# Kernel tuning notes

Measured on AMD Instinct MI355X. Metric: run time of the kernel, lower is better.

## Reference

```python
import jax, jax.numpy as jnp
import numpy as np

N_NODES = 50000
N_EDGES = 800000
IN_DIM = 128
HIDDEN = 256
N_CLASSES = 16
N_GRAPHS = 128


def setup_inputs() -> dict:
    key = jax.random.key(0)
    ks = jax.random.split(key, 10)
    x = jax.random.normal(ks[0], (N_NODES, IN_DIM), dtype=jnp.float32)
    edge_index = jax.random.randint(ks[1], (2, N_EDGES), 0, N_NODES, dtype=jnp.int64)
    batch = jnp.sort(jax.random.randint(ks[2], (N_NODES,), 0, N_GRAPHS, dtype=jnp.int64))
    s = 1.0 / np.sqrt(HIDDEN)
    return {
        "x": x,
        "edge_index": edge_index,
        "batch": batch,
        "W_in": jax.random.normal(ks[3], (IN_DIM, HIDDEN), dtype=jnp.float32) / np.sqrt(IN_DIM),
        "b_in": jnp.zeros((HIDDEN,), dtype=jnp.float32),
        "W1": jax.random.normal(ks[4], (HIDDEN, HIDDEN), dtype=jnp.float32) * s,
        "b1": jnp.zeros((HIDDEN,), dtype=jnp.float32),
        "W2": jax.random.normal(ks[5], (HIDDEN, HIDDEN), dtype=jnp.float32) * s,
        "b2": jnp.zeros((HIDDEN,), dtype=jnp.float32),
        "W_out": jax.random.normal(ks[6], (HIDDEN, N_CLASSES), dtype=jnp.float32) * s,
        "b_out": jnp.zeros((N_CLASSES,), dtype=jnp.float32),
    }


def gcn_conv(x, W, b, src, dst):
    # PyG GCNConv: add self-loops, symmetric norm D^-1/2 A D^-1/2, scatter-add at target.
    h = x @ W  # [N, H]
    n = x.shape[0]
    # degree of target nodes, including one self-loop per node
    deg = jax.ops.segment_sum(jnp.ones_like(dst, dtype=h.dtype), dst, num_segments=n) + 1.0
    dinv = deg ** -0.5  # [N]
    norm = dinv[src] * dinv[dst]  # [E]
    msg = h[src] * norm[:, None]  # [E, H]  gather + scale
    agg = jax.ops.segment_sum(msg, dst, num_segments=n)  # scatter-add
    agg = agg + h * (dinv * dinv)[:, None]  # self-loop contribution
    return agg + b


def reference(x, edge_index, batch, W_in, b_in, W1, b1, W2, b2, W_out, b_out):
    src, dst = edge_index[0], edge_index[1]
    h = x @ W_in + b_in
    # layer 1 (dropout is identity in eval mode)
    h = jax.nn.relu(gcn_conv(h, W1, b1, src, dst))
    # layer 2
    h = jax.nn.relu(gcn_conv(h, W2, b2, src, dst))
    # global mean pool over graphs
    sums = jax.ops.segment_sum(h, batch, num_segments=N_GRAPHS)  # [G, H]
    counts = jax.ops.segment_sum(jnp.ones((h.shape[0],), h.dtype), batch, num_segments=N_GRAPHS)
    pooled = sums / jnp.maximum(counts, 1.0)[:, None]
    return pooled @ W_out + b_out  # [G, n_classes]
```

## Files before the change

kernel.cpp:

```cpp
#include <hip/hip_runtime.h>
#include <hip/hip_bf16.h>

typedef __attribute__((ext_vector_type(8))) short bf16x8;
typedef __attribute__((ext_vector_type(4))) float f32x4;
typedef __attribute__((ext_vector_type(8))) unsigned short u16x8;

__device__ __forceinline__ unsigned short f2bf(float f) {
    unsigned u = __float_as_uint(f);
    u += 0x7fff + ((u >> 16) & 1);
    return (unsigned short)(u >> 16);
}
__device__ __forceinline__ float bf2f(unsigned short s) {
    return __uint_as_float(((unsigned)s) << 16);
}

#define GL2LDS16(g, l) __builtin_amdgcn_global_load_lds(                      \
        (const __attribute__((address_space(1))) void*)(g),                   \
        (__attribute__((address_space(3))) void*)(l), 16, 0, 0)


__global__ __launch_bounds__(256) void fused_misc_kernel(
        const int* __restrict__ dst, int* __restrict__ cnt, int e,
        const float* __restrict__ W2, unsigned short* __restrict__ Wt2,
        const float* __restrict__ x, unsigned short* __restrict__ xb, int n4,
        int CB, int TB) {
    int b = blockIdx.x;
    if (b < CB) {
        int i = b * 256 + threadIdx.x;
        if (i < e) atomicAdd(&cnt[dst[i]], 1);
    } else if (b < CB + TB) {
        int i = (b - CB) * 256 + threadIdx.x;
        int k = i >> 8, n = i & 255;
        Wt2[(size_t)n * 256 + k] = f2bf(W2[i]);
    } else {
        int i = (b - CB - TB) * 256 + threadIdx.x;
        if (i < n4) {
            float4 v = ((const float4*)x)[i];
            ushort4 o;
            o.x = f2bf(v.x); o.y = f2bf(v.y); o.z = f2bf(v.z); o.w = f2bf(v.w);
            ((ushort4*)xb)[i] = o;
        }
    }
}


__global__ __launch_bounds__(256) void wfuse_kernel(const float* __restrict__ W_in,
                                                    const float* __restrict__ b_in,
                                                    const float* __restrict__ W1,
                                                    unsigned short* __restrict__ WfT,
                                                    float* __restrict__ bv) {
    __shared__ float row[256];
    int k = blockIdx.x;
    int n = threadIdx.x;
    row[n] = (k < 128) ? W_in[k * 256 + n] : b_in[n];
    __syncthreads();
    float acc = 0.f;
    #pragma unroll 4
    for (int j = 0; j < 256; ++j) acc = fmaf(row[j], W1[j * 256 + n], acc);
    if (k < 128) WfT[(size_t)n * 128 + k] = f2bf(acc);
    else bv[n] = acc;
}


__global__ __launch_bounds__(256) void block_sum_kernel(const int* __restrict__ cnt,
                                                        int* __restrict__ bsums, int n) {
    int tid = threadIdx.x;
    int i = blockIdx.x * 256 + tid;
    int v = (i < n) ? cnt[i] : 0;
    #pragma unroll
    for (int off = 32; off > 0; off >>= 1) v += __shfl_down(v, off);
    __shared__ int ws[4];
    if ((tid & 63) == 0) ws[tid >> 6] = v;
    __syncthreads();
    if (tid == 0) bsums[blockIdx.x] = ws[0] + ws[1] + ws[2] + ws[3];
}

__global__ __launch_bounds__(256) void scatter_scan_kernel(const int* __restrict__ cnt,
                                                           const int* __restrict__ bsums,
                                                           int* __restrict__ offsets,
                                                           int* __restrict__ cursor,
                                                           float* __restrict__ dinv,
                                                           int n, int nb) {
    int tid = threadIdx.x;
    int lane = tid & 63, wid = tid >> 6;
    __shared__ int ws[4], wp[4];

    int bv = (tid < nb && tid < (int)blockIdx.x) ? bsums[tid] : 0;
    int br = bv;
    #pragma unroll
    for (int off = 32; off > 0; off >>= 1) br += __shfl_down(br, off);
    if (lane == 0) wp[wid] = br;

    int i = blockIdx.x * 256 + tid;
    int v = (i < n) ? cnt[i] : 0;
    int s = v;
    #pragma unroll
    for (int off = 1; off < 64; off <<= 1) {
        int t = __shfl_up(s, off);
        if (lane >= off) s += t;
    }
    if (lane == 63) ws[wid] = s;
    __syncthreads();
    int wo = 0;
    #pragma unroll
    for (int k = 0; k < 4; ++k) wo += (k < wid) ? ws[k] : 0;
    int bpref = wp[0] + wp[1] + wp[2] + wp[3];
    int excl = bpref + wo + s - v;
    if (i <= n) { offsets[i] = excl; }
    if (i < n) {
        cursor[i] = excl;
        dinv[i] = rsqrtf((float)v + 1.0f);
    }
}

__global__ void fill_kernel(const int* __restrict__ src, const int* __restrict__ dst,
                            int* __restrict__ cursor, int* __restrict__ csr, int e) {
    int i = blockIdx.x * blockDim.x + threadIdx.x;
    if (i < e) {
        int p = atomicAdd(&cursor[dst[i]], 1);
        csr[p] = src[i];
    }
}


template <int MODE>
__global__ __launch_bounds__(256) void gemm_bf16(const unsigned short* __restrict__ A,
                                                 const unsigned short* __restrict__ Wt,
                                                 const float* __restrict__ aux,
                                                 const float* __restrict__ aux2,
                                                 const float* __restrict__ aux3,
                                                 unsigned short* __restrict__ C,
                                                 int M, int K) {
    __shared__ unsigned short As[128 * 64];
    __shared__ unsigned short Bs[128 * 64];
    const int tid  = threadIdx.x;
    const int lane = tid & 63;
    const int w    = tid >> 6;
    const int wr   = w >> 1, wc = w & 1;
    const int row0 = blockIdx.x * 128;
    const int col0 = blockIdx.y * 128;
    const int mlane = lane & 15, quad = lane >> 4;

    f32x4 acc[4][4];
    #pragma unroll
    for (int i = 0; i < 4; ++i)
        #pragma unroll
        for (int j = 0; j < 4; ++j) acc[i][j] = f32x4{0.f, 0.f, 0.f, 0.f};

    const unsigned short* gA[4]; const unsigned short* gB[4];
    unsigned short* lA[4]; unsigned short* lB[4];
    #pragma unroll
    for (int p = 0; p < 4; ++p) {
        int cid = (p * 4 + w) * 64 + lane;
        int row = cid >> 3, slot = cid & 7;
        int rowA = row0 + row; if (rowA >= M) rowA = M - 1;
        gA[p] = A + (size_t)rowA * K + slot * 8;
        gB[p] = Wt + (size_t)(col0 + row) * K + slot * 8;
        lA[p] = &As[((p * 4 + w) * 64) * 8];
        lB[p] = &Bs[((p * 4 + w) * 64) * 8];
    }

    for (int k0 = 0; k0 < K; k0 += 64) {
        #pragma unroll
        for (int p = 0; p < 4; ++p) GL2LDS16(gA[p] + k0, lA[p]);
        #pragma unroll
        for (int p = 0; p < 4; ++p) GL2LDS16(gB[p] + k0, lB[p]);
        __syncthreads();
        #pragma unroll
        for (int ks = 0; ks < 2; ++ks) {
            bf16x8 af[4], bfv[4];
            #pragma unroll
            for (int i = 0; i < 4; ++i)
                af[i] = *(const bf16x8*)&As[(wr * 64 + i * 16 + mlane) * 64 + ks * 32 + quad * 8];
            #pragma unroll
            for (int j = 0; j < 4; ++j)
                bfv[j] = *(const bf16x8*)&Bs[(wc * 64 + j * 16 + mlane) * 64 + ks * 32 + quad * 8];
            #pragma unroll
            for (int i = 0; i < 4; ++i)
                #pragma unroll
                for (int j = 0; j < 4; ++j)
                    acc[i][j] = __builtin_amdgcn_mfma_f32_16x16x32_bf16(af[i], bfv[j], acc[i][j], 0, 0, 0);
        }
        __syncthreads();
    }

    float bj[4], cj[4];
    if (MODE == 0) {
        #pragma unroll
        for (int j = 0; j < 4; ++j) bj[j] = aux[col0 + wc * 64 + j * 16 + mlane];
    } else if (MODE == 2) {
        #pragma unroll
        for (int j = 0; j < 4; ++j) {
            int gcol = col0 + wc * 64 + j * 16 + mlane;
            bj[j] = aux2[gcol];
            cj[j] = aux3[gcol];
        }
    }
    #pragma unroll
    for (int i = 0; i < 4; ++i) {
        #pragma unroll
        for (int r = 0; r < 4; ++r) {
            int grow = row0 + wr * 64 + i * 16 + quad * 4 + r;
            if (grow < M) {
                float d = (MODE != 0) ? aux[grow] : 0.f;
                #pragma unroll
                for (int j = 0; j < 4; ++j) {
                    int gcol = col0 + wc * 64 + j * 16 + mlane;
                    float v = acc[i][j][r];
                    if (MODE == 0)      v = v + bj[j];
                    else if (MODE == 1) v = v * d;
                    else {              v = fmaf(d, bj[j], v) + cj[j]; v = fmaxf(v, 0.f); }
                    C[(size_t)grow * 256 + gcol] = f2bf(v);
                }
            }
        }
    }
}


__global__ __launch_bounds__(256) void agg_x_kernel(const unsigned short* __restrict__ xb,
                                                    const int* __restrict__ offsets,
                                                    const int* __restrict__ csr,
                                                    const float* __restrict__ dinv,
                                                    unsigned short* __restrict__ ax,
                                                    float* __restrict__ s_out, int n) {
    int node = blockIdx.x * 4 + (threadIdx.x >> 6);
    if (node >= n) return;
    int lane = threadIdx.x & 63;
    int q = lane >> 4, hl = lane & 15;
    const u16x8* x8 = (const u16x8*)xb;
    int beg = offsets[node], end = offsets[node + 1];
    float dn = dinv[node];
    float acc[8] = {0.f,0.f,0.f,0.f,0.f,0.f,0.f,0.f};
    float acc2[8] = {0.f,0.f,0.f,0.f,0.f,0.f,0.f,0.f};
    float sdl = 0.f;

    int e = beg;
    while (e < end) {
        int cnt = end - e; if (cnt > 64) cnt = 64;
        int myi = 0; float mydv = 0.f;
        if (lane < cnt) { myi = csr[e + lane]; mydv = dinv[myi]; sdl += mydv; }
        for (int j = 0; j < cnt; j += 32) {
            int s[8]; float w[8]; u16x8 v[8];
            #pragma unroll
            for (int k = 0; k < 8; ++k) {
                int slot = j + 4 * k + q;
                s[k] = __shfl(myi, slot);
                w[k] = __shfl(mydv, slot);
            }
            #pragma unroll
            for (int k = 0; k < 8; ++k) v[k] = x8[(size_t)s[k] * 16 + hl];
            #pragma unroll
            for (int k = 0; k < 8; k += 2) {
                #pragma unroll
                for (int c = 0; c < 8; ++c) acc[c]  = fmaf(bf2f(v[k][c]),   w[k],   acc[c]);
                #pragma unroll
                for (int c = 0; c < 8; ++c) acc2[c] = fmaf(bf2f(v[k+1][c]), w[k+1], acc2[c]);
            }
        }
        e += cnt;
    }
    #pragma unroll
    for (int c = 0; c < 8; ++c) {
        acc[c] += acc2[c];
        acc[c] += __shfl_xor(acc[c], 16);
        acc[c] += __shfl_xor(acc[c], 32);
    }
    float sd = sdl;
    #pragma unroll
    for (int off = 32; off > 0; off >>= 1) sd += __shfl_down(sd, off);
    if (lane < 16) {
        u16x8 sv = x8[(size_t)node * 16 + hl];
        u16x8 r;
        #pragma unroll
        for (int c = 0; c < 8; ++c) {
            float v = fmaf(dn, bf2f(sv[c]), acc[c]) * dn;
            r[c] = f2bf(v);
        }
        ((u16x8*)ax)[(size_t)node * 16 + hl] = r;
        if (lane == 0) s_out[node] = dn * (sd + dn);
    }
}


__global__ __launch_bounds__(256) void agg_kernel(const unsigned short* __restrict__ hs,
                                                  const int* __restrict__ offsets,
                                                  const int* __restrict__ csr,
                                                  const float* __restrict__ dinv,
                                                  const float* __restrict__ bias,
                                                  unsigned short* __restrict__ out, int n) {
    int node = blockIdx.x * 4 + (threadIdx.x >> 6);
    if (node >= n) return;
    int lane = threadIdx.x & 63;
    int half = lane >> 5, hl = lane & 31;
    const u16x8* hs8 = (const u16x8*)hs;
    int beg = offsets[node], end = offsets[node + 1];
    float acc[8] = {0.f,0.f,0.f,0.f,0.f,0.f,0.f,0.f};
    float acc2[8] = {0.f,0.f,0.f,0.f,0.f,0.f,0.f,0.f};

    int e = beg;
    while (e < end) {
        int cnt = end - e; if (cnt > 64) cnt = 64;
        int myi = (lane < cnt) ? csr[e + lane] : 0;
        for (int j = 0; j < cnt; j += 16) {
            int s[8]; float w[8]; u16x8 v[8];
            #pragma unroll
            for (int k = 0; k < 8; ++k) {
                int slot = j + 2 * k + half;
                s[k] = __shfl(myi, slot);
                w[k] = (slot < cnt) ? 1.0f : 0.0f;
            }
            #pragma unroll
            for (int k = 0; k < 8; ++k) v[k] = hs8[(size_t)s[k] * 32 + hl];
            #pragma unroll
            for (int k = 0; k < 8; k += 2) {
                #pragma unroll
                for (int c = 0; c < 8; ++c) acc[c]  = fmaf(bf2f(v[k][c]),   w[k],   acc[c]);
                #pragma unroll
                for (int c = 0; c < 8; ++c) acc2[c] = fmaf(bf2f(v[k+1][c]), w[k+1], acc2[c]);
            }
        }
        e += cnt;
    }
    #pragma unroll
    for (int c = 0; c < 8; ++c) {
        acc[c] += acc2[c];
        acc[c] += __shfl_xor(acc[c], 32);
    }
    if (lane < 32) {
        u16x8 sv = hs8[(size_t)node * 32 + hl];
        float d = dinv[node];
        float4 b0 = ((const float4*)bias)[hl * 2];
        float4 b1 = ((const float4*)bias)[hl * 2 + 1];
        float bb[8] = {b0.x, b0.y, b0.z, b0.w, b1.x, b1.y, b1.z, b1.w};
        u16x8 r;
        #pragma unroll
        for (int c = 0; c < 8; ++c) {
            float v = fmaf(acc[c] + bf2f(sv[c]), d, bb[c]);
            r[c] = f2bf(fmaxf(v, 0.f));
        }
        ((u16x8*)out)[(size_t)node * 32 + hl] = r;
    }
}


__global__ __launch_bounds__(256) void pool_partial_kernel(const unsigned short* __restrict__ h,
                                                           const int* __restrict__ batch,
                                                           float* __restrict__ sums,
                                                           int* __restrict__ counts,
                                                           int n, int chunk) {
    int beg = blockIdx.x * chunk;
    int end = beg + chunk; if (end > n) end = n;
    if (beg >= end) return;
    int c = threadIdx.x;
    int curg = batch[beg];
    float acc = 0.f;
    int runlen = 0;
    for (int i = beg; i < end; ++i) {
        int g = batch[i];
        if (g != curg) {
            atomicAdd(&sums[(size_t)curg * 256 + c], acc);
            if (c == 0) atomicAdd(&counts[curg], runlen);
            acc = 0.f; runlen = 0; curg = g;
        }
        acc += bf2f(h[(size_t)i * 256 + c]);
        ++runlen;
    }
    atomicAdd(&sums[(size_t)curg * 256 + c], acc);
    if (c == 0) atomicAdd(&counts[curg], runlen);
}

__global__ __launch_bounds__(256) void pool_final_kernel(const float* __restrict__ sums,
                                                         const int* __restrict__ counts,
                                                         const float* __restrict__ Wout,
                                                         const float* __restrict__ bout,
                                                         float* __restrict__ out) {
    __shared__ float pl[256];
    int g = blockIdx.x;
    int c = threadIdx.x;
    int cnt = counts[g];
    pl[c] = sums[(size_t)g * 256 + c] / (float)(cnt > 0 ? cnt : 1);
    __syncthreads();
    if (c < 16) {
        float o = bout[c];
        #pragma unroll 4
        for (int k = 0; k < 256; ++k) o = fmaf(pl[k], Wout[k * 16 + c], o);
        out[g * 16 + c] = o;
    }
}


extern "C" void kernel_launch(void* const* d_in, const int* in_sizes, int n_in,
                              void* d_out, int out_size, void* d_ws, size_t ws_size,
                              hipStream_t stream) {
    const float* x     = (const float*)d_in[0];
    const int*   ei    = (const int*)d_in[1];
    const int*   batch = (const int*)d_in[2];
    const float* W_in  = (const float*)d_in[3];
    const float* b_in  = (const float*)d_in[4];
    const float* W1    = (const float*)d_in[5];
    const float* b1    = (const float*)d_in[6];
    const float* W2    = (const float*)d_in[7];
    const float* b2    = (const float*)d_in[8];
    const float* Wout  = (const float*)d_in[9];
    const float* bout  = (const float*)d_in[10];

    const int E = in_sizes[1] / 2;
    const int N = in_sizes[2];
    const int IN_DIM = in_sizes[0] / N;
    const int G = 128;
    const int* src = ei;
    const int* dst = ei + E;

    char* ws = (char*)d_ws;
    size_t off = 0;
    auto alloc = [&](size_t bytes) { size_t p = off; off += (bytes + 255) & ~(size_t)255; return p; };
    unsigned short* bufA = (unsigned short*)(ws + alloc((size_t)N * 256 * 2));
    unsigned short* bufB = (unsigned short*)(ws + alloc((size_t)N * 256 * 2));
    unsigned short* xb   = (unsigned short*)(ws + alloc((size_t)N * IN_DIM * 2));
    unsigned short* Wt2  = (unsigned short*)(ws + alloc((size_t)256 * 256 * 2));
    unsigned short* WfT  = (unsigned short*)(ws + alloc((size_t)256 * IN_DIM * 2));
    float*          bv   = (float*)(ws + alloc((size_t)256 * 4));
    float*          sbuf = (float*)(ws + alloc((size_t)N * 4));
    size_t zbeg = off;
    int*   deg_cnt = (int*)(ws + alloc((size_t)N * 4));
    float* sums    = (float*)(ws + alloc((size_t)G * 256 * 4));
    int*   counts  = (int*)(ws + alloc((size_t)G * 4));
    size_t zend = off;
    float* dinv    = (float*)(ws + alloc((size_t)N * 4));
    int*   offsets = (int*)(ws + alloc((size_t)(N + 1) * 4));
    int*   cursor  = (int*)(ws + alloc((size_t)N * 4));
    int*   csr     = (int*)(ws + alloc((size_t)E * 4));
    int*   bsums   = (int*)(ws + alloc((size_t)256 * 4));
    (void)ws_size;

    unsigned short* axb = bufB;

    const int NB  = (N + 255) / 256;
    const int NB1 = (N + 1 + 255) / 256;
    const int CB  = (E + 255) / 256;
    const int TB  = (256 * 256 + 255) / 256;
    const int XB  = (N * IN_DIM / 4 + 255) / 256;

    hipMemsetAsync(ws + zbeg, 0, zend - zbeg, stream);
    fused_misc_kernel<<<CB + TB + XB, 256, 0, stream>>>(
        dst, deg_cnt, E, W2, Wt2, x, xb, N * IN_DIM / 4, CB, TB);
    wfuse_kernel<<<129, 256, 0, stream>>>(W_in, b_in, W1, WfT, bv);
    block_sum_kernel<<<NB, 256, 0, stream>>>(deg_cnt, bsums, N);
    scatter_scan_kernel<<<NB1, 256, 0, stream>>>(deg_cnt, bsums, offsets, cursor, dinv, N, NB);
    fill_kernel<<<(E + 255) / 256, 256, 0, stream>>>(src, dst, cursor, csr, E);

    agg_x_kernel<<<(N + 3) / 4, 256, 0, stream>>>(xb, offsets, csr, dinv, axb, sbuf, N);
    dim3 gg((N + 127) / 128, 2);
    gemm_bf16<2><<<gg, 256, 0, stream>>>(axb, WfT, sbuf, bv, b1, bufA, N, IN_DIM);

    gemm_bf16<1><<<gg, 256, 0, stream>>>(bufA, Wt2, dinv, nullptr, nullptr, bufB, N, 256);
    agg_kernel<<<(N + 3) / 4, 256, 0, stream>>>(bufB, offsets, csr, dinv, b2, bufA, N);

    const int PBLOCKS = 512;
    int chunk = (N + PBLOCKS - 1) / PBLOCKS;
    pool_partial_kernel<<<PBLOCKS, 256, 0, stream>>>(bufA, batch, sums, counts, N, chunk);
    pool_final_kernel<<<G, 256, 0, stream>>>(sums, counts, Wout, bout, (float*)d_out);
}
```

Measured before the change: 387.0 us.

## Fuse layer-2 aggregation with mean-pool atomics and merge setup kernels

The second GCN aggregation now adds each node's ReLU output straight into per-graph sums with float atomics, so the intermediate node-feature buffer is never written and the separate pool_partial pass is gone. The aggregation is restructured so each lane covers four features and neighbors are processed eight at a time. The weight-fusion kernel and a per-graph node count are folded into the misc setup launch, removing launches. The price is heavy atomic contention: each node issues 256 atomics into only 128 graph rows, and the float summation order becomes nondeterministic.

```diff
diff --git a/kernel.cpp b/kernel.cpp
--- a/kernel.cpp
+++ b/kernel.cpp
@@ -23,16 +23,21 @@
         const int* __restrict__ dst, int* __restrict__ cnt, int e,
         const float* __restrict__ W2, unsigned short* __restrict__ Wt2,
         const float* __restrict__ x, unsigned short* __restrict__ xb, int n4,
-        int CB, int TB) {
+        const float* __restrict__ W_in, const float* __restrict__ b_in,
+        const float* __restrict__ W1,
+        unsigned short* __restrict__ WfT, float* __restrict__ bv,
+        const int* __restrict__ batch, int* __restrict__ counts, int n,
+        int CB, int TB, int XB, int WB) {
+    __shared__ float row[256];
     int b = blockIdx.x;
     if (b < CB) {
         int i = b * 256 + threadIdx.x;
         if (i < e) atomicAdd(&cnt[dst[i]], 1);
     } else if (b < CB + TB) {
         int i = (b - CB) * 256 + threadIdx.x;
-        int k = i >> 8, n = i & 255;
-        Wt2[(size_t)n * 256 + k] = f2bf(W2[i]);
-    } else {
+        int k = i >> 8, nn = i & 255;
+        Wt2[(size_t)nn * 256 + k] = f2bf(W2[i]);
+    } else if (b < CB + TB + XB) {
         int i = (b - CB - TB) * 256 + threadIdx.x;
         if (i < n4) {
             float4 v = ((const float4*)x)[i];
@@ -40,25 +45,20 @@
             o.x = f2bf(v.x); o.y = f2bf(v.y); o.z = f2bf(v.z); o.w = f2bf(v.w);
             ((ushort4*)xb)[i] = o;
         }
-    }
-}
-
-
-__global__ __launch_bounds__(256) void wfuse_kernel(const float* __restrict__ W_in,
-                                                    const float* __restrict__ b_in,
-                                                    const float* __restrict__ W1,
-                                                    unsigned short* __restrict__ WfT,
-                                                    float* __restrict__ bv) {
-    __shared__ float row[256];
-    int k = blockIdx.x;
-    int n = threadIdx.x;
-    row[n] = (k < 128) ? W_in[k * 256 + n] : b_in[n];
-    __syncthreads();
-    float acc = 0.f;
-    #pragma unroll 4
-    for (int j = 0; j < 256; ++j) acc = fmaf(row[j], W1[j * 256 + n], acc);
-    if (k < 128) WfT[(size_t)n * 128 + k] = f2bf(acc);
-    else bv[n] = acc;
+    } else if (b < CB + TB + XB + WB) {
+        int k = b - (CB + TB + XB);
+        int nn = threadIdx.x;
+        row[nn] = (k < 128) ? W_in[k * 256 + nn] : b_in[nn];
+        __syncthreads();
+        float acc = 0.f;
+        #pragma unroll 4
+        for (int j = 0; j < 256; ++j) acc = fmaf(row[j], W1[j * 256 + nn], acc);
+        if (k < 128) WfT[(size_t)nn * 128 + k] = f2bf(acc);
+        else bv[nn] = acc;
+    } else {
+        int i = (b - CB - TB - XB - WB) * 256 + threadIdx.x;
+        if (i < n) atomicAdd(&counts[batch[i]], 1);
+    }
 }
 
 
@@ -283,92 +283,72 @@
 }
 
 
-__global__ __launch_bounds__(256) void agg_kernel(const unsigned short* __restrict__ hs,
-                                                  const int* __restrict__ offsets,
-                                                  const int* __restrict__ csr,
-                                                  const float* __restrict__ dinv,
-                                                  const float* __restrict__ bias,
-                                                  unsigned short* __restrict__ out, int n) {
+__global__ __launch_bounds__(256) void agg_pool_kernel(const unsigned short* __restrict__ hs,
+                                                       const int* __restrict__ offsets,
+                                                       const int* __restrict__ csr,
+                                                       const float* __restrict__ dinv,
+                                                       const float* __restrict__ bias,
+                                                       const int* __restrict__ batch,
+                                                       float* __restrict__ sums, int n) {
     int node = blockIdx.x * 4 + (threadIdx.x >> 6);
     if (node >= n) return;
     int lane = threadIdx.x & 63;
-    int half = lane >> 5, hl = lane & 31;
-    const u16x8* hs8 = (const u16x8*)hs;
+    const ushort4* hs4 = (const ushort4*)hs;
     int beg = offsets[node], end = offsets[node + 1];
-    float acc[8] = {0.f,0.f,0.f,0.f,0.f,0.f,0.f,0.f};
-    float acc2[8] = {0.f,0.f,0.f,0.f,0.f,0.f,0.f,0.f};
+    ushort4 sv = hs4[(size_t)node * 64 + lane];
+    float a0 = bf2f(sv.x), a1 = bf2f(sv.y), a2 = bf2f(sv.z), a3 = bf2f(sv.w);
+    float c0 = 0.f, c1 = 0.f, c2 = 0.f, c3 = 0.f;
 
     int e = beg;
     while (e < end) {
         int cnt = end - e; if (cnt > 64) cnt = 64;
         int myi = (lane < cnt) ? csr[e + lane] : 0;
-        for (int j = 0; j < cnt; j += 16) {
-            int s[8]; float w[8]; u16x8 v[8];
-            #pragma unroll
-            for (int k = 0; k < 8; ++k) {
-                int slot = j + 2 * k + half;
-                s[k] = __shfl(myi, slot);
-                w[k] = (slot < cnt) ? 1.0f : 0.0f;
-            }
-            #pragma unroll
-            for (int k = 0; k < 8; ++k) v[k] = hs8[(size_t)s[k] * 32 + hl];
-            #pragma unroll
-            for (int k = 0; k < 8; k += 2) {
-                #pragma unroll
-                for (int c = 0; c < 8; ++c) acc[c]  = fmaf(bf2f(v[k][c]),   w[k],   acc[c]);
-                #pragma unroll
-                for (int c = 0; c < 8; ++c) acc2[c] = fmaf(bf2f(v[k+1][c]), w[k+1], acc2[c]);
-            }
+        int j = 0;
+        for (; j + 8 <= cnt; j += 8) {
+            int s0 = __shfl(myi, j + 0), s1 = __shfl(myi, j + 1);
+            int s2 = __shfl(myi, j + 2), s3 = __shfl(myi, j + 3);
+            int s4 = __shfl(myi, j + 4), s5 = __shfl(myi, j + 5);
+            int s6 = __shfl(myi, j + 6), s7 = __shfl(myi, j + 7);
+            ushort4 v0 = hs4[(size_t)s0 * 64 + lane];
+            ushort4 v1 = hs4[(size_t)s1 * 64 + lane];
+            ushort4 v2 = hs4[(size_t)s2 * 64 + lane];
+            ushort4 v3 = hs4[(size_t)s3 * 64 + lane];
+            ushort4 v4 = hs4[(size_t)s4 * 64 + lane];
+            ushort4 v5 = hs4[(size_t)s5 * 64 + lane];
+            ushort4 v6 = hs4[(size_t)s6 * 64 + lane];
+            ushort4 v7 = hs4[(size_t)s7 * 64 + lane];
+            a0 += bf2f(v0.x) + bf2f(v1.x) + bf2f(v2.x) + bf2f(v3.x);
+            a1 += bf2f(v0.y) + bf2f(v1.y) + bf2f(v2.y) + bf2f(v3.y);
+            a2 += bf2f(v0.z) + bf2f(v1.z) + bf2f(v2.z) + bf2f(v3.z);
+            a3 += bf2f(v0.w) + bf2f(v1.w) + bf2f(v2.w) + bf2f(v3.w);
+            c0 += bf2f(v4.x) + bf2f(v5.x) + bf2f(v6.x) + bf2f(v7.x);
+            c1 += bf2f(v4.y) + bf2f(v5.y) + bf2f(v6.y) + bf2f(v7.y);
+            c2 += bf2f(v4.z) + bf2f(v5.z) + bf2f(v6.z) + bf2f(v7.z);
+            c3 += bf2f(v4.w) + bf2f(v5.w) + bf2f(v6.w) + bf2f(v7.w);
+        }
+        for (; j < cnt; ++j) {
+            int s = __shfl(myi, j);
+            ushort4 v = hs4[(size_t)s * 64 + lane];
+            a0 += bf2f(v.x); a1 += bf2f(v.y); a2 += bf2f(v.z); a3 += bf2f(v.w);
         }
         e += cnt;
     }
-    #pragma unroll
-    for (int c = 0; c < 8; ++c) {
-        acc[c] += acc2[c];
-        acc[c] += __shfl_xor(acc[c], 32);
-    }
-    if (lane < 32) {
-        u16x8 sv = hs8[(size_t)node * 32 + hl];
-        float d = dinv[node];
-        float4 b0 = ((const float4*)bias)[hl * 2];
-        float4 b1 = ((const float4*)bias)[hl * 2 + 1];
-        float bb[8] = {b0.x, b0.y, b0.z, b0.w, b1.x, b1.y, b1.z, b1.w};
-        u16x8 r;
-        #pragma unroll
-        for (int c = 0; c < 8; ++c) {
-            float v = fmaf(acc[c] + bf2f(sv[c]), d, bb[c]);
-            r[c] = f2bf(fmaxf(v, 0.f));
-        }
-        ((u16x8*)out)[(size_t)node * 32 + hl] = r;
-    }
-}
-
-
-__global__ __launch_bounds__(256) void pool_partial_kernel(const unsigned short* __restrict__ h,
-                                                           const int* __restrict__ batch,
-                                                           float* __restrict__ sums,
-                                                           int* __restrict__ counts,
-                                                           int n, int chunk) {
-    int beg = blockIdx.x * chunk;
-    int end = beg + chunk; if (end > n) end = n;
-    if (beg >= end) return;
-    int c = threadIdx.x;
-    int curg = batch[beg];
-    float acc = 0.f;
-    int runlen = 0;
-    for (int i = beg; i < end; ++i) {
-        int g = batch[i];
-        if (g != curg) {
-            atomicAdd(&sums[(size_t)curg * 256 + c], acc);
-            if (c == 0) atomicAdd(&counts[curg], runlen);
-            acc = 0.f; runlen = 0; curg = g;
-        }
-        acc += bf2f(h[(size_t)i * 256 + c]);
-        ++runlen;
-    }
-    atomicAdd(&sums[(size_t)curg * 256 + c], acc);
-    if (c == 0) atomicAdd(&counts[curg], runlen);
-}
+    a0 += c0; a1 += c1; a2 += c2; a3 += c3;
+
+    float d = dinv[node];
+    float4 b = ((const float4*)bias)[lane];
+    float r0 = fmaxf(fmaf(a0, d, b.x), 0.f);
+    float r1 = fmaxf(fmaf(a1, d, b.y), 0.f);
+    float r2 = fmaxf(fmaf(a2, d, b.z), 0.f);
+    float r3 = fmaxf(fmaf(a3, d, b.w), 0.f);
+    int g = batch[node];
+    float* sp = &sums[(size_t)g * 256 + lane * 4];
+    atomicAdd(sp + 0, r0);
+    atomicAdd(sp + 1, r1);
+    atomicAdd(sp + 2, r2);
+    atomicAdd(sp + 3, r3);
+}
+
 
 __global__ __launch_bounds__(256) void pool_final_kernel(const float* __restrict__ sums,
                                                          const int* __restrict__ counts,
@@ -441,11 +421,13 @@
     const int CB  = (E + 255) / 256;
     const int TB  = (256 * 256 + 255) / 256;
     const int XB  = (N * IN_DIM / 4 + 255) / 256;
+    const int WB  = 129;
 
     hipMemsetAsync(ws + zbeg, 0, zend - zbeg, stream);
-    fused_misc_kernel<<<CB + TB + XB, 256, 0, stream>>>(
-        dst, deg_cnt, E, W2, Wt2, x, xb, N * IN_DIM / 4, CB, TB);
-    wfuse_kernel<<<129, 256, 0, stream>>>(W_in, b_in, W1, WfT, bv);
+    fused_misc_kernel<<<CB + TB + XB + WB + NB, 256, 0, stream>>>(
+        dst, deg_cnt, E, W2, Wt2, x, xb, N * IN_DIM / 4,
+        W_in, b_in, W1, WfT, bv, batch, counts, N,
+        CB, TB, XB, WB);
     block_sum_kernel<<<NB, 256, 0, stream>>>(deg_cnt, bsums, N);
     scatter_scan_kernel<<<NB1, 256, 0, stream>>>(deg_cnt, bsums, offsets, cursor, dinv, N, NB);
     fill_kernel<<<(E + 255) / 256, 256, 0, stream>>>(src, dst, cursor, csr, E);
@@ -455,10 +437,7 @@
     gemm_bf16<2><<<gg, 256, 0, stream>>>(axb, WfT, sbuf, bv, b1, bufA, N, IN_DIM);
 
     gemm_bf16<1><<<gg, 256, 0, stream>>>(bufA, Wt2, dinv, nullptr, nullptr, bufB, N, 256);
-    agg_kernel<<<(N + 3) / 4, 256, 0, stream>>>(bufB, offsets, csr, dinv, b2, bufA, N);
-
-    const int PBLOCKS = 512;
-    int chunk = (N + PBLOCKS - 1) / PBLOCKS;
-    pool_partial_kernel<<<PBLOCKS, 256, 0, stream>>>(bufA, batch, sums, counts, N, chunk);
+    agg_pool_kernel<<<(N + 3) / 4, 256, 0, stream>>>(bufB, offsets, csr, dinv, b2, batch, sums, N);
+
     pool_final_kernel<<<G, 256, 0, stream>>>(sums, counts, Wout, bout, (float*)d_out);
 }
```

After: 665.3 us. +71.9%, slower.
